# Optimization experiments

Measured on AMD Instinct MI355X. Metric: run time of the kernel, lower is better.

The kernel has to match this reference:

```python
import jax, jax.numpy as jnp
import numpy as np

N = 65536      # flattened latent vectors (e.g. 64 images x 32x32 latents)
K = 1024       # num_embeddings (codebook size)
D = 64         # latent_dim


def setup_inputs() -> dict:
    key = jax.random.key(0)
    k_x, k_e = jax.random.split(key)
    inputs = jax.random.normal(k_x, (N, D), dtype=jnp.float32)
    # codebook initialized ~ tf.random_normal_initializer (stddev=0.05)
    embeddings = jax.random.normal(k_e, (K, D), dtype=jnp.float32) * 0.05
    return {"inputs": inputs, "embeddings": embeddings}


def reference(inputs, embeddings):
    # Pairwise L2 distances ||x_n - e_k||_2 -> [N, K].
    x_sq = jnp.sum(inputs * inputs, axis=-1, keepdims=True)        # [N, 1]
    e_sq = jnp.sum(embeddings * embeddings, axis=-1)               # [K]
    cross = inputs @ embeddings.T                                   # [N, K]
    sq_dist = x_sq + e_sq[None, :] - 2.0 * cross                    # [N, K]
    return jnp.sqrt(jnp.maximum(sq_dist, 0.0))
```

## Files before the change

### kernel.cpp

```cpp
#include <hip/hip_runtime.h>


typedef __attribute__((ext_vector_type(8))) short short8;
typedef __attribute__((ext_vector_type(4))) float floatx4;

#define LSTR 72

__device__ inline unsigned short f2bf(float f) {
    unsigned int u = __float_as_uint(f);
    u += 0x7FFFu + ((u >> 16) & 1u);
    return (unsigned short)(u >> 16);
}
__device__ inline float bf2f(unsigned short h) {
    return __uint_as_float(((unsigned int)h) << 16);
}

__global__ __launch_bounds__(256) void vq_dist(const float* __restrict__ X,
                                               const float* __restrict__ E,
                                               float* __restrict__ out,
                                               int Ktot) {
    __shared__ unsigned short lA[128 * LSTR];
    __shared__ unsigned short lB[128 * LSTR];
    __shared__ float s_xsq[128];
    __shared__ float s_esq[128];

    const int tid = threadIdx.x;
    const size_t m0 = (size_t)blockIdx.y * 128;
    const int n0 = blockIdx.x * 128;

    {
        const int r8 = tid >> 3;
        const int c8 = (tid & 7) * 8;
        #pragma unroll
        for (int it = 0; it < 4; ++it) {
            const int row = it * 32 + r8;
            {
                const float* src = X + (m0 + row) * 64 + c8;
                float4 v0 = *(const float4*)src;
                float4 v1 = *(const float4*)(src + 4);
                unsigned short h[8] = {f2bf(v0.x), f2bf(v0.y), f2bf(v0.z), f2bf(v0.w),
                                       f2bf(v1.x), f2bf(v1.y), f2bf(v1.z), f2bf(v1.w)};
                float s = 0.f;
                short8 pk;
                #pragma unroll
                for (int j = 0; j < 8; ++j) {
                    float f = bf2f(h[j]);
                    s = fmaf(f, f, s);
                    pk[j] = (short)h[j];
                }
                *(short8*)&lA[row * LSTR + c8] = pk;
                s += __shfl_down(s, 4, 8);
                s += __shfl_down(s, 2, 8);
                s += __shfl_down(s, 1, 8);
                if ((tid & 7) == 0) s_xsq[row] = s;
            }
            {
                const float* src = E + (size_t)(n0 + row) * 64 + c8;
                float4 v0 = *(const float4*)src;
                float4 v1 = *(const float4*)(src + 4);
                unsigned short h[8] = {f2bf(v0.x), f2bf(v0.y), f2bf(v0.z), f2bf(v0.w),
                                       f2bf(v1.x), f2bf(v1.y), f2bf(v1.z), f2bf(v1.w)};
                float s = 0.f;
                short8 pk;
                #pragma unroll
                for (int j = 0; j < 8; ++j) {
                    float f = bf2f(h[j]);
                    s = fmaf(f, f, s);
                    pk[j] = (short)h[j];
                }
                *(short8*)&lB[row * LSTR + c8] = pk;
                s += __shfl_down(s, 4, 8);
                s += __shfl_down(s, 2, 8);
                s += __shfl_down(s, 1, 8);
                if ((tid & 7) == 0) s_esq[row] = s;
            }
        }
    }
    __syncthreads();

    const int w = tid >> 6;
    const int lane = tid & 63;
    const int quad = lane >> 4;
    const int l16 = lane & 15;
    const int wm = (w >> 1) * 64;
    const int wn = (w & 1) * 64;

    short8 a0[4], a1[4], b0[4], b1[4];
    #pragma unroll
    for (int t = 0; t < 4; ++t) {
        const int ar = wm + t * 16 + l16;
        a0[t] = *(const short8*)&lA[ar * LSTR + quad * 8];
        a1[t] = *(const short8*)&lA[ar * LSTR + 32 + quad * 8];
        const int br = wn + t * 16 + l16;
        b0[t] = *(const short8*)&lB[br * LSTR + quad * 8];
        b1[t] = *(const short8*)&lB[br * LSTR + 32 + quad * 8];
    }

    floatx4 acc[4][4];
    #pragma unroll
    for (int i = 0; i < 4; ++i)
        #pragma unroll
        for (int j = 0; j < 4; ++j)
            acc[i][j] = (floatx4){0.f, 0.f, 0.f, 0.f};

    #pragma unroll
    for (int i = 0; i < 4; ++i)
        #pragma unroll
        for (int j = 0; j < 4; ++j) {
            acc[i][j] = __builtin_amdgcn_mfma_f32_16x16x32_bf16(a0[i], b0[j], acc[i][j], 0, 0, 0);
            acc[i][j] = __builtin_amdgcn_mfma_f32_16x16x32_bf16(a1[i], b1[j], acc[i][j], 0, 0, 0);
        }

    #pragma unroll
    for (int i = 0; i < 4; ++i) {
        const int mrow = wm + i * 16 + quad * 4;
        float xq[4];
        #pragma unroll
        for (int r = 0; r < 4; ++r) xq[r] = s_xsq[mrow + r];
        #pragma unroll
        for (int j = 0; j < 4; ++j) {
            const int ncol = wn + j * 16 + l16;
            const float eq = s_esq[ncol];
            float* op = out + (m0 + mrow) * Ktot + (n0 + ncol);
            #pragma unroll
            for (int r = 0; r < 4; ++r) {
                float d = xq[r] + eq - 2.0f * acc[i][j][r];
                d = fmaxf(d, 0.0f);
                op[(size_t)r * Ktot] = sqrtf(d);
            }
        }
    }
}

extern "C" void kernel_launch(void* const* d_in, const int* in_sizes, int n_in,
                              void* d_out, int out_size, void* d_ws, size_t ws_size,
                              hipStream_t stream) {
    const float* X = (const float*)d_in[0];
    const float* E = (const float*)d_in[1];
    float* out = (float*)d_out;
    const int N = in_sizes[0] / 64;
    const int K = in_sizes[1] / 64;
    dim3 grid(K / 128, N / 128);
    vq_dist<<<grid, dim3(256), 0, stream>>>(X, E, out, K);
}
```

Measured before the change: 328.1 us.

## Split bf16 conversion into prep kernel and DMA tiles directly to LDS

Adds a prep kernel that converts X and E to padded bf16 once and precomputes row squared norms into the workspace. The main kernel then copies the pre-converted tiles straight into LDS with global_load_lds instead of converting per block. This removes the repeated fp32 loads and conversions each tile did (X was converted once per column block). Output stores become nontemporal. It costs an extra launch plus an extra round trip of the bf16 copy through memory, and it hardcodes N and K.

```diff
diff --git a/kernel.cpp b/kernel.cpp
--- a/kernel.cpp
+++ b/kernel.cpp
@@ -4,82 +4,104 @@
 typedef __attribute__((ext_vector_type(8))) short short8;
 typedef __attribute__((ext_vector_type(4))) float floatx4;
 
+typedef __attribute__((address_space(3))) unsigned int lds_u32;
+typedef __attribute__((address_space(1))) const unsigned int glb_u32;
+
 #define LSTR 72
+#define N_ROWS 65536
+#define K_ROWS 1024
 
-__device__ inline unsigned short f2bf(float f) {
+#define WS_XB  0u
+#define WS_EB  9437184u
+#define WS_XSQ 9584640u
+#define WS_ESQ 9846784u
+
+__device__ __forceinline__ unsigned short f2bf(float f) {
     unsigned int u = __float_as_uint(f);
     u += 0x7FFFu + ((u >> 16) & 1u);
     return (unsigned short)(u >> 16);
 }
-__device__ inline float bf2f(unsigned short h) {
+__device__ __forceinline__ float bf2f(unsigned short h) {
     return __uint_as_float(((unsigned int)h) << 16);
 }
 
-__global__ __launch_bounds__(256) void vq_dist(const float* __restrict__ X,
+__global__ __launch_bounds__(256) void vq_prep(const float* __restrict__ X,
                                                const float* __restrict__ E,
+                                               unsigned short* __restrict__ Xb,
+                                               unsigned short* __restrict__ Eb,
+                                               float* __restrict__ xsq,
+                                               float* __restrict__ esq) {
+    const int t = blockIdx.x * 256 + threadIdx.x;
+    const int row = t >> 3;
+    const int c8 = (t & 7) * 8;
+    const float* src;
+    unsigned short* dst;
+    float* sq;
+    int r;
+    if (row < N_ROWS) {
+        r = row;
+        src = X + (size_t)r * 64 + c8;
+        dst = Xb + (size_t)r * LSTR + c8;
+        sq = xsq;
+    } else {
+        r = row - N_ROWS;
+        src = E + (size_t)r * 64 + c8;
+        dst = Eb + (size_t)r * LSTR + c8;
+        sq = esq;
+    }
+    float4 v0 = *(const float4*)src;
+    float4 v1 = *(const float4*)(src + 4);
+    unsigned short h[8] = {f2bf(v0.x), f2bf(v0.y), f2bf(v0.z), f2bf(v0.w),
+                           f2bf(v1.x), f2bf(v1.y), f2bf(v1.z), f2bf(v1.w)};
+    float s = 0.f;
+    short8 pk;
+    #pragma unroll
+    for (int j = 0; j < 8; ++j) {
+        float f = bf2f(h[j]);
+        s = fmaf(f, f, s);
+        pk[j] = (short)h[j];
+    }
+    *(short8*)dst = pk;
+    s += __shfl_down(s, 4, 8);
+    s += __shfl_down(s, 2, 8);
+    s += __shfl_down(s, 1, 8);
+    if ((t & 7) == 0) sq[r] = s;
+}
+
+__global__ __launch_bounds__(256) void vq_main(const unsigned short* __restrict__ Xb,
+                                               const unsigned short* __restrict__ Eb,
+                                               const float* __restrict__ xsq,
+                                               const float* __restrict__ esq,
                                                float* __restrict__ out,
                                                int Ktot) {
-    __shared__ unsigned short lA[128 * LSTR];
-    __shared__ unsigned short lB[128 * LSTR];
+    __shared__ unsigned short lds[2 * 128 * LSTR];
     __shared__ float s_xsq[128];
     __shared__ float s_esq[128];
 
     const int tid = threadIdx.x;
+    const int w = tid >> 6;
+    const int lane = tid & 63;
     const size_t m0 = (size_t)blockIdx.y * 128;
     const int n0 = blockIdx.x * 128;
 
-    {
-        const int r8 = tid >> 3;
-        const int c8 = (tid & 7) * 8;
-        #pragma unroll
-        for (int it = 0; it < 4; ++it) {
-            const int row = it * 32 + r8;
-            {
-                const float* src = X + (m0 + row) * 64 + c8;
-                float4 v0 = *(const float4*)src;
-                float4 v1 = *(const float4*)(src + 4);
-                unsigned short h[8] = {f2bf(v0.x), f2bf(v0.y), f2bf(v0.z), f2bf(v0.w),
-                                       f2bf(v1.x), f2bf(v1.y), f2bf(v1.z), f2bf(v1.w)};
-                float s = 0.f;
-                short8 pk;
-                #pragma unroll
-                for (int j = 0; j < 8; ++j) {
-                    float f = bf2f(h[j]);
-                    s = fmaf(f, f, s);
-                    pk[j] = (short)h[j];
-                }
-                *(short8*)&lA[row * LSTR + c8] = pk;
-                s += __shfl_down(s, 4, 8);
-                s += __shfl_down(s, 2, 8);
-                s += __shfl_down(s, 1, 8);
-                if ((tid & 7) == 0) s_xsq[row] = s;
-            }
-            {
-                const float* src = E + (size_t)(n0 + row) * 64 + c8;
-                float4 v0 = *(const float4*)src;
-                float4 v1 = *(const float4*)(src + 4);
-                unsigned short h[8] = {f2bf(v0.x), f2bf(v0.y), f2bf(v0.z), f2bf(v0.w),
-                                       f2bf(v1.x), f2bf(v1.y), f2bf(v1.z), f2bf(v1.w)};
-                float s = 0.f;
-                short8 pk;
-                #pragma unroll
-                for (int j = 0; j < 8; ++j) {
-                    float f = bf2f(h[j]);
-                    s = fmaf(f, f, s);
-                    pk[j] = (short)h[j];
-                }
-                *(short8*)&lB[row * LSTR + c8] = pk;
-                s += __shfl_down(s, 4, 8);
-                s += __shfl_down(s, 2, 8);
-                s += __shfl_down(s, 1, 8);
-                if ((tid & 7) == 0) s_esq[row] = s;
-            }
-        }
+    const char* srcA = (const char*)(Xb + m0 * LSTR);
+    const char* srcB = (const char*)(Eb + (size_t)n0 * LSTR);
+    #pragma unroll
+    for (int c = 0; c < 9; ++c) {
+        const int chunk = w * 9 + c;
+        const int off = chunk * 1024 + lane * 16;
+        const char* g = (chunk < 18) ? (srcA + off) : (srcB + (off - 18432));
+        __builtin_amdgcn_global_load_lds((glb_u32*)g,
+                                         (lds_u32*)((char*)lds + chunk * 1024),
+                                         16, 0, 0);
     }
+    if (tid < 128) s_xsq[tid] = xsq[m0 + tid];
+    else           s_esq[tid - 128] = esq[n0 + tid - 128];
     __syncthreads();
 
-    const int w = tid >> 6;
-    const int lane = tid & 63;
+    const unsigned short* lA = lds;
+    const unsigned short* lB = lds + 128 * LSTR;
+
     const int quad = lane >> 4;
     const int l16 = lane & 15;
     const int wm = (w >> 1) * 64;
@@ -126,7 +148,7 @@
             for (int r = 0; r < 4; ++r) {
                 float d = xq[r] + eq - 2.0f * acc[i][j][r];
                 d = fmaxf(d, 0.0f);
-                op[(size_t)r * Ktot] = sqrtf(d);
+                __builtin_nontemporal_store(sqrtf(d), op + (size_t)r * Ktot);
             }
         }
     }
@@ -138,8 +160,16 @@
     const float* X = (const float*)d_in[0];
     const float* E = (const float*)d_in[1];
     float* out = (float*)d_out;
-    const int N = in_sizes[0] / 64;
     const int K = in_sizes[1] / 64;
-    dim3 grid(K / 128, N / 128);
-    vq_dist<<<grid, dim3(256), 0, stream>>>(X, E, out, K);
+
+    char* ws = (char*)d_ws;
+    unsigned short* Xb = (unsigned short*)(ws + WS_XB);
+    unsigned short* Eb = (unsigned short*)(ws + WS_EB);
+    float* xsq = (float*)(ws + WS_XSQ);
+    float* esq = (float*)(ws + WS_ESQ);
+
+    vq_prep<<<dim3((N_ROWS + K_ROWS) * 8 / 256), dim3(256), 0, stream>>>(X, E, Xb, Eb, xsq, esq);
+
+    dim3 grid(K / 128, N_ROWS / 128);
+    vq_main<<<grid, dim3(256), 0, stream>>>(Xb, Eb, xsq, esq, out, K);
 }
```

After: 309.1 us. 1.06x faster.
